# Optimization experiments

Hardware: AMD Instinct MI355X
Metric: run time of the kernel (lower is better)

Reference implementation:

```python
import jax, jax.numpy as jnp
import numpy as np


def setup_inputs() -> dict:
    key = jax.random.key(0)
    ks = jax.random.split(key, 7)
    B, S, IN, OUT = 4, 2048, 4096, 4096
    R_DEC, R_TR = 1024, 64
    return {
        "x": jax.random.normal(ks[0], (B, S, IN), dtype=jnp.float32),
        "siva_u_t": jax.random.normal(ks[1], (OUT, R_TR), dtype=jnp.float32) * 0.02,
        "siva_u_d": jax.random.normal(ks[2], (OUT, R_DEC - R_TR), dtype=jnp.float32) * 0.02,
        "siva_s": jax.random.uniform(ks[3], (R_DEC,), dtype=jnp.float32),
        "siva_v_t": jax.random.normal(ks[4], (R_TR, IN), dtype=jnp.float32) * 0.02,
        "siva_v_d": jax.random.normal(ks[5], (R_DEC - R_TR, IN), dtype=jnp.float32) * 0.02,
        "bias": jax.random.normal(ks[6], (OUT,), dtype=jnp.float32) * 0.02,
    }


def reference(x, siva_u_t, siva_u_d, siva_s, siva_v_t, siva_v_d, bias):
    # Faithful to torch: weight = (cat(U_t, U_d, dim=1) * S) @ cat(V_t, V_d, dim=0)
    siva_u = jnp.concatenate((siva_u_t, siva_u_d), axis=1)   # [out, r]
    siva_v = jnp.concatenate((siva_v_t, siva_v_d), axis=0)   # [r, in]
    weight = (siva_u * siva_s) @ siva_v                       # [out, in]
    # F.linear: x @ weight.T + bias
    return jnp.einsum("bsi,oi->bso", x, weight) + bias
```

## Files before the change

kernel.cpp:

```cpp
#include <hip/hip_runtime.h>
#include <cstdint>


typedef __bf16 bf16x8 __attribute__((ext_vector_type(8)));
typedef float f32x4 __attribute__((ext_vector_type(4)));

__device__ __forceinline__ unsigned short f32_to_bf16(float f) {
    union { float f; uint32_t u; } v; v.f = f;
    uint32_t u = v.u;
    u += 0x7FFF + ((u >> 16) & 1);
    return (unsigned short)(u >> 16);
}

__global__ void cast_f32_bf16(const float* __restrict__ src,
                              unsigned short* __restrict__ dst, int n4) {
    int i = blockIdx.x * blockDim.x + threadIdx.x;
    if (i >= n4) return;
    float4 v = ((const float4*)src)[i];
    ushort4 o;
    o.x = f32_to_bf16(v.x); o.y = f32_to_bf16(v.y);
    o.z = f32_to_bf16(v.z); o.w = f32_to_bf16(v.w);
    ((ushort4*)dst)[i] = o;
}

__global__ void build_u(const float* __restrict__ u_t, const float* __restrict__ u_d,
                        const float* __restrict__ s, unsigned short* __restrict__ ub,
                        int n4) {
    int i = blockIdx.x * blockDim.x + threadIdx.x;
    if (i >= n4) return;
    int e = i * 4;
    int o = e >> 10;
    int r = e & 1023;
    float4 u;
    if (r < 64) u = *(const float4*)(u_t + (size_t)o * 64 + r);
    else        u = *(const float4*)(u_d + (size_t)o * 960 + (r - 64));
    float4 sv = *(const float4*)(s + r);
    ushort4 w;
    w.x = f32_to_bf16(u.x * sv.x);
    w.y = f32_to_bf16(u.y * sv.y);
    w.z = f32_to_bf16(u.z * sv.z);
    w.w = f32_to_bf16(u.w * sv.w);
    ((ushort4*)ub)[i] = w;
}

__global__ void reduce_y(const float* __restrict__ p0, const float* __restrict__ p1,
                         unsigned short* __restrict__ y, int n4) {
    int i = blockIdx.x * blockDim.x + threadIdx.x;
    if (i >= n4) return;
    float4 a = ((const float4*)p0)[i];
    float4 b = ((const float4*)p1)[i];
    ushort4 w;
    w.x = f32_to_bf16(a.x + b.x);
    w.y = f32_to_bf16(a.y + b.y);
    w.z = f32_to_bf16(a.z + b.z);
    w.w = f32_to_bf16(a.w + b.w);
    ((ushort4*)y)[i] = w;
}

__device__ __forceinline__ void stage16(const unsigned short* g, unsigned short* l) {
    __builtin_amdgcn_global_load_lds(
        (const __attribute__((address_space(1))) uint32_t*)g,
        (__attribute__((address_space(3))) uint32_t*)l, 16, 0, 0);
}


#define STAGE_A(bb, kh, t_) do {                                              \
    const unsigned short* s_ = pAsrc + (t_) * 64 + (kh) * 32;                 \
    unsigned short* d_ = ldsA_dst + (bb) * 32768 + (kh) * 8192;               \
    stage16(s_, d_);                                                          \
    stage16(s_ + (size_t)128 * LD, d_ + 4096);                                \
} while (0)

#define STAGE_B(bb, kh, t_) do {                                              \
    const unsigned short* s_ = pBsrc + (t_) * 64 + (kh) * 32;                 \
    unsigned short* d_ = ldsB_dst + (bb) * 32768 + (kh) * 8192;               \
    stage16(s_, d_);                                                          \
    stage16(s_ + (size_t)128 * LD, d_ + 4096);                                \
} while (0)

#define READ_AF(bb, ks, mh) do {                                              \
    const unsigned short* p_ = lds + (bb) * 32768 + (ks) * 8192 + aoff + (mh) * 2048; \
    af[0] = *(const bf16x8*)(p_);                                             \
    af[1] = *(const bf16x8*)(p_ + 512);                                       \
    af[2] = *(const bf16x8*)(p_ + 1024);                                      \
    af[3] = *(const bf16x8*)(p_ + 1536);                                      \
} while (0)

#define READ_BF(bb, ks) do {                                                  \
    const unsigned short* p_ = lds + (bb) * 32768 + 16384 + (ks) * 8192 + boff; \
    bfr[0] = *(const bf16x8*)(p_);                                            \
    bfr[1] = *(const bf16x8*)(p_ + 512);                                      \
    bfr[2] = *(const bf16x8*)(p_ + 1024);                                     \
    bfr[3] = *(const bf16x8*)(p_ + 1536);                                     \
} while (0)

#define MFMA16(mh) do {                                                       \
    __builtin_amdgcn_s_barrier();                                             \
    __builtin_amdgcn_sched_barrier(0);                                        \
    __builtin_amdgcn_s_setprio(1);                                            \
    _Pragma("unroll") for (int i_ = 0; i_ < 4; ++i_) {                        \
        _Pragma("unroll") for (int n_ = 0; n_ < 4; ++n_) {                    \
            acc[(mh) * 4 + i_][n_] = __builtin_amdgcn_mfma_f32_16x16x32_bf16( \
                af[i_], bfr[n_], acc[(mh) * 4 + i_][n_], 0, 0, 0);            \
        }                                                                     \
    }                                                                         \
    __builtin_amdgcn_s_setprio(0);                                            \
    __builtin_amdgcn_sched_barrier(0);                                        \
} while (0)

#define PHASE_END do {                                                        \
    __builtin_amdgcn_s_barrier();                                             \
    __builtin_amdgcn_sched_barrier(0);                                        \
} while (0)

#define BODY(t_, bb) do {                                                     \
    const int tp1 = (t_) + 1, tp2 = (t_) + 2;                                 \
    bf16x8 af[4], bfr[4];                                                     \
                                                          \
    READ_AF(bb, 0, 0); READ_BF(bb, 0);                                        \
    if (tp1 < KTILES) STAGE_A((bb) ^ 1, 1, tp1);                              \
    MFMA16(0); PHASE_END;                                                     \
                                                          \
    READ_AF(bb, 0, 1);                                                        \
    if (tp1 < KTILES) STAGE_B((bb) ^ 1, 1, tp1);                              \
    MFMA16(1); PHASE_END;                                                     \
                                                          \
    READ_AF(bb, 1, 0); READ_BF(bb, 1);                                        \
    if (tp2 < KTILES) STAGE_A((bb), 0, tp2);                                  \
    MFMA16(0); PHASE_END;                                                     \
                                                          \
    READ_AF(bb, 1, 1);                                                        \
    if (tp2 < KTILES) STAGE_B((bb), 0, tp2);                                  \
    MFMA16(1);                                                                \
    if (tp2 < KTILES)      asm volatile("s_waitcnt vmcnt(4)" ::: "memory");   \
    else if (tp1 < KTILES) asm volatile("s_waitcnt vmcnt(0)" ::: "memory");   \
    PHASE_END;                                                                \
} while (0)

template<int KTILES, int LD, int NTX, bool BIAS, int SPLITK>
__global__ __launch_bounds__(512, 2)
void gemm256(const unsigned short* __restrict__ A, const unsigned short* __restrict__ B,
             float* __restrict__ C, const float* __restrict__ bias) {
    static_assert((KTILES % 2) == 0 && KTILES >= 4, "KTILES even >= 4");
    __shared__ unsigned short lds[65536];

    const int tid = threadIdx.x;
    const int wv = tid >> 6, lane = tid & 63;
    const int wm = wv >> 2, wn = wv & 3;
    const int q = lane >> 4, l16 = lane & 15;

    const int cpx = gridDim.x >> 3;
    const int bswz = (blockIdx.x & 7) * cpx + (blockIdx.x >> 3);
    const int tx = bswz % NTX, ty = bswz / NTX;
    const int m0 = ty * 256, n0 = tx * 256;

    const int z = blockIdx.z;
    const unsigned short* Az = A + (size_t)z * SPLITK;
    const unsigned short* Bz = B + (size_t)z * SPLITK;
    float* Cz = C + (size_t)z * 8192 * (NTX * 256);

    const int rowS = tid >> 2;
    const int ccS  = (tid & 3) ^ ((tid >> 3) & 3);
    const unsigned short* pAsrc = Az + (size_t)(m0 + rowS) * LD + ccS * 8;
    const unsigned short* pBsrc = Bz + (size_t)(n0 + rowS) * LD + ccS * 8;
    unsigned short* ldsA_dst = lds + tid * 8;
    unsigned short* ldsB_dst = lds + 16384 + tid * 8;

    const int xr = (l16 >> 1) & 3;
    const int qx = (q ^ xr) * 8;
    const int aoff = (wm * 128 + l16) * 32 + qx;
    const int boff = (wn * 64 + l16) * 32 + qx;

    f32x4 acc[8][4] = {};

    STAGE_A(0, 0, 0); STAGE_B(0, 0, 0);
    STAGE_A(0, 1, 0); STAGE_B(0, 1, 0);
    STAGE_A(1, 0, 1); STAGE_B(1, 0, 1);
    asm volatile("s_waitcnt vmcnt(4)" ::: "memory");
    __builtin_amdgcn_s_barrier();
    __builtin_amdgcn_sched_barrier(0);

    for (int t = 0; t < KTILES; t += 2) {
        BODY(t, 0);
        BODY(t + 1, 1);
    }

    const int ldc = NTX * 256;
    float bvv[4];
    if (BIAS) {
#pragma unroll
        for (int nf = 0; nf < 4; ++nf) bvv[nf] = bias[n0 + wn * 64 + nf * 16 + l16];
    }
#pragma unroll
    for (int mf = 0; mf < 8; ++mf) {
#pragma unroll
        for (int nf = 0; nf < 4; ++nf) {
            const int col = n0 + wn * 64 + nf * 16 + l16;
            const size_t rb = (size_t)(m0 + wm * 128 + mf * 16 + q * 4);
#pragma unroll
            for (int i = 0; i < 4; ++i) {
                float v = acc[mf][nf][i];
                if (BIAS) v += bvv[nf];
                Cz[(rb + i) * ldc + col] = v;
            }
        }
    }
}

extern "C" void kernel_launch(void* const* d_in, const int* in_sizes, int n_in,
                              void* d_out, int out_size, void* d_ws, size_t ws_size,
                              hipStream_t stream) {
    const float* x    = (const float*)d_in[0];
    const float* u_t  = (const float*)d_in[1];
    const float* u_d  = (const float*)d_in[2];
    const float* s    = (const float*)d_in[3];
    const float* v_t  = (const float*)d_in[4];
    const float* v_d  = (const float*)d_in[5];
    const float* bias = (const float*)d_in[6];
    float* out = (float*)d_out;

    const int M = 8192, IN = 4096, R = 1024, OUT = 4096;

    char* ws = (char*)d_ws;
    float*          Yp = (float*)ws;
    unsigned short* xb = (unsigned short*)(ws + (size_t)(64 << 20));
    unsigned short* Vb = (unsigned short*)(ws + (size_t)(128 << 20));
    unsigned short* Ub = (unsigned short*)(ws + (size_t)(136 << 20));
    unsigned short* Yb = (unsigned short*)(ws + (size_t)(144 << 20));

    {
        int n4 = M * IN / 4;
        cast_f32_bf16<<<(n4 + 255) / 256, 256, 0, stream>>>(x, xb, n4);
    }
    {
        int n4 = 64 * IN / 4;
        cast_f32_bf16<<<(n4 + 255) / 256, 256, 0, stream>>>(v_t, Vb, n4);
    }
    {
        int n4 = 960 * IN / 4;
        cast_f32_bf16<<<(n4 + 255) / 256, 256, 0, stream>>>(v_d, Vb + 64 * IN, n4);
    }
    {
        int n4 = OUT * R / 4;
        build_u<<<(n4 + 255) / 256, 256, 0, stream>>>(u_t, u_d, s, Ub, n4);
    }

    gemm256<32, 4096, 4, false, 2048><<<dim3(128, 1, 2), 512, 0, stream>>>(xb, Vb, Yp, nullptr);
    {
        int n4 = M * R / 4;
        reduce_y<<<(n4 + 255) / 256, 256, 0, stream>>>(Yp, Yp + (size_t)M * R, Yb, n4);
    }
    gemm256<16, 1024, 16, true, 0><<<dim3(512, 1, 1), 512, 0, stream>>>(Yb, Ub, out, bias);
}
```

Baseline: 413.9 us.

## Replace split-K first GEMM with 128x256-tile kernel writing bf16 directly

The first GEMM (x @ V^T) previously used split-K over 2 with fp32 partial outputs and a separate reduce kernel. It now uses a dedicated 128x256 tile kernel with 256 blocks over the full K, writing bf16 directly. This removes the fp32 partial round trip and one launch, and the workspace layout is compacted to match. The vmcnt wait counts in the 256-tile GEMM are also retuned so more loads stay in flight. The risks are a smaller tile with less data reuse and a waitcnt scheme that could be wrong.

```diff
diff --git a/kernel.cpp b/kernel.cpp
--- a/kernel.cpp
+++ b/kernel.cpp
@@ -43,26 +43,11 @@
     ((ushort4*)ub)[i] = w;
 }
 
-__global__ void reduce_y(const float* __restrict__ p0, const float* __restrict__ p1,
-                         unsigned short* __restrict__ y, int n4) {
-    int i = blockIdx.x * blockDim.x + threadIdx.x;
-    if (i >= n4) return;
-    float4 a = ((const float4*)p0)[i];
-    float4 b = ((const float4*)p1)[i];
-    ushort4 w;
-    w.x = f32_to_bf16(a.x + b.x);
-    w.y = f32_to_bf16(a.y + b.y);
-    w.z = f32_to_bf16(a.z + b.z);
-    w.w = f32_to_bf16(a.w + b.w);
-    ((ushort4*)y)[i] = w;
-}
-
 __device__ __forceinline__ void stage16(const unsigned short* g, unsigned short* l) {
     __builtin_amdgcn_global_load_lds(
         (const __attribute__((address_space(1))) uint32_t*)g,
         (__attribute__((address_space(3))) uint32_t*)l, 16, 0, 0);
 }
-
 
 #define STAGE_A(bb, kh, t_) do {                                              \
     const unsigned short* s_ = pAsrc + (t_) * 64 + (kh) * 32;                 \
@@ -123,7 +108,10 @@
                                                           \
     READ_AF(bb, 0, 1);                                                        \
     if (tp1 < KTILES) STAGE_B((bb) ^ 1, 1, tp1);                              \
-    MFMA16(1); PHASE_END;                                                     \
+    MFMA16(1);                                                                \
+    if (tp1 < KTILES) asm volatile("s_waitcnt vmcnt(8)" ::: "memory");        \
+    else              asm volatile("s_waitcnt vmcnt(0)" ::: "memory");        \
+    PHASE_END;                                                                \
                                                           \
     READ_AF(bb, 1, 0); READ_BF(bb, 1);                                        \
     if (tp2 < KTILES) STAGE_A((bb), 0, tp2);                                  \
@@ -132,12 +120,12 @@
     READ_AF(bb, 1, 1);                                                        \
     if (tp2 < KTILES) STAGE_B((bb), 0, tp2);                                  \
     MFMA16(1);                                                                \
-    if (tp2 < KTILES)      asm volatile("s_waitcnt vmcnt(4)" ::: "memory");   \
-    else if (tp1 < KTILES) asm volatile("s_waitcnt vmcnt(0)" ::: "memory");   \
+    if (tp2 < KTILES)      asm volatile("s_waitcnt vmcnt(8)" ::: "memory");   \
+    else if (tp1 < KTILES) asm volatile("s_waitcnt vmcnt(4)" ::: "memory");   \
     PHASE_END;                                                                \
 } while (0)
 
-template<int KTILES, int LD, int NTX, bool BIAS, int SPLITK>
+template<int KTILES, int LD, int NTX, bool BIAS>
 __global__ __launch_bounds__(512, 2)
 void gemm256(const unsigned short* __restrict__ A, const unsigned short* __restrict__ B,
              float* __restrict__ C, const float* __restrict__ bias) {
@@ -154,15 +142,10 @@
     const int tx = bswz % NTX, ty = bswz / NTX;
     const int m0 = ty * 256, n0 = tx * 256;
 
-    const int z = blockIdx.z;
-    const unsigned short* Az = A + (size_t)z * SPLITK;
-    const unsigned short* Bz = B + (size_t)z * SPLITK;
-    float* Cz = C + (size_t)z * 8192 * (NTX * 256);
-
     const int rowS = tid >> 2;
     const int ccS  = (tid & 3) ^ ((tid >> 3) & 3);
-    const unsigned short* pAsrc = Az + (size_t)(m0 + rowS) * LD + ccS * 8;
-    const unsigned short* pBsrc = Bz + (size_t)(n0 + rowS) * LD + ccS * 8;
+    const unsigned short* pAsrc = A + (size_t)(m0 + rowS) * LD + ccS * 8;
+    const unsigned short* pBsrc = B + (size_t)(n0 + rowS) * LD + ccS * 8;
     unsigned short* ldsA_dst = lds + tid * 8;
     unsigned short* ldsB_dst = lds + 16384 + tid * 8;
 
@@ -176,7 +159,7 @@
     STAGE_A(0, 0, 0); STAGE_B(0, 0, 0);
     STAGE_A(0, 1, 0); STAGE_B(0, 1, 0);
     STAGE_A(1, 0, 1); STAGE_B(1, 0, 1);
-    asm volatile("s_waitcnt vmcnt(4)" ::: "memory");
+    asm volatile("s_waitcnt vmcnt(8)" ::: "memory");
     __builtin_amdgcn_s_barrier();
     __builtin_amdgcn_sched_barrier(0);
 
@@ -201,8 +184,118 @@
             for (int i = 0; i < 4; ++i) {
                 float v = acc[mf][nf][i];
                 if (BIAS) v += bvv[nf];
-                Cz[(rb + i) * ldc + col] = v;
+                C[(rb + i) * ldc + col] = v;
             }
+        }
+    }
+}
+
+#define ST2_A(bb, kh, t_)                                                     \
+    stage16(pAsrc + (t_) * 64 + (kh) * 32, lds + (bb) * 24576 + (kh) * 4096 + tid * 8)
+
+#define ST2_B(bb, kh, t_) do {                                                \
+    const unsigned short* s_ = pBsrc + (t_) * 64 + (kh) * 32;                 \
+    unsigned short* d_ = lds + (bb) * 24576 + 8192 + (kh) * 8192 + tid * 8;   \
+    stage16(s_, d_);                                                          \
+    stage16(s_ + (size_t)128 * 4096, d_ + 4096);                              \
+} while (0)
+
+#define RD2_A(bb, ks) do {                                                    \
+    const unsigned short* p_ = lds + (bb) * 24576 + (ks) * 4096 + aoff;       \
+    af[0] = *(const bf16x8*)(p_);                                             \
+    af[1] = *(const bf16x8*)(p_ + 512);                                       \
+    af[2] = *(const bf16x8*)(p_ + 1024);                                      \
+    af[3] = *(const bf16x8*)(p_ + 1536);                                      \
+} while (0)
+
+#define RD2_B(bb, ks) do {                                                    \
+    const unsigned short* p_ = lds + (bb) * 24576 + 8192 + (ks) * 8192 + boff; \
+    bfr[0] = *(const bf16x8*)(p_);                                            \
+    bfr[1] = *(const bf16x8*)(p_ + 512);                                      \
+    bfr[2] = *(const bf16x8*)(p_ + 1024);                                     \
+    bfr[3] = *(const bf16x8*)(p_ + 1536);                                     \
+} while (0)
+
+#define MM16 do {                                                             \
+    __builtin_amdgcn_s_barrier();                                             \
+    __builtin_amdgcn_sched_barrier(0);                                        \
+    __builtin_amdgcn_s_setprio(1);                                            \
+    _Pragma("unroll") for (int i_ = 0; i_ < 4; ++i_) {                        \
+        _Pragma("unroll") for (int n_ = 0; n_ < 4; ++n_) {                    \
+            acc[i_][n_] = __builtin_amdgcn_mfma_f32_16x16x32_bf16(            \
+                af[i_], bfr[n_], acc[i_][n_], 0, 0, 0);                       \
+        }                                                                     \
+    }                                                                         \
+    __builtin_amdgcn_s_setprio(0);                                            \
+    __builtin_amdgcn_sched_barrier(0);                                        \
+} while (0)
+
+#define BODY2(t_, bb) do {                                                    \
+    const int tp1 = (t_) + 1, tp2 = (t_) + 2;                                 \
+    bf16x8 af[4], bfr[4];                                                     \
+                                                                \
+    RD2_A(bb, 0); RD2_B(bb, 0);                                               \
+    if (tp1 < 64) { ST2_A((bb) ^ 1, 1, tp1); ST2_B((bb) ^ 1, 1, tp1); }       \
+    MM16;                                                                     \
+    if (tp1 < 64) asm volatile("s_waitcnt vmcnt(6)" ::: "memory");            \
+    else          asm volatile("s_waitcnt vmcnt(0)" ::: "memory");            \
+    PHASE_END;                                                                \
+                                                                \
+    RD2_A(bb, 1); RD2_B(bb, 1);                                               \
+    if (tp2 < 64) { ST2_A((bb), 0, tp2); ST2_B((bb), 0, tp2); }               \
+    MM16;                                                                     \
+    if (tp2 < 64)      asm volatile("s_waitcnt vmcnt(6)" ::: "memory");       \
+    else if (tp1 < 64) asm volatile("s_waitcnt vmcnt(3)" ::: "memory");       \
+    PHASE_END;                                                                \
+} while (0)
+
+__global__ __launch_bounds__(512, 2)
+void gemm_a128(const unsigned short* __restrict__ A, const unsigned short* __restrict__ B,
+               unsigned short* __restrict__ Y) {
+    __shared__ unsigned short lds[49152];
+
+    const int tid = threadIdx.x;
+    const int wv = tid >> 6, lane = tid & 63;
+    const int wm = wv >> 2, wn = wv & 3;
+    const int q = lane >> 4, l16 = lane & 15;
+
+    const int bswz = (blockIdx.x & 7) * 32 + (blockIdx.x >> 3);
+    const int tx = bswz & 3, ty = bswz >> 2;
+    const int m0 = ty * 128, n0 = tx * 256;
+
+    const int rowS = tid >> 2;
+    const int ccS  = (tid & 3) ^ ((tid >> 3) & 3);
+    const unsigned short* pAsrc = A + (size_t)(m0 + rowS) * 4096 + ccS * 8;
+    const unsigned short* pBsrc = B + (size_t)(n0 + rowS) * 4096 + ccS * 8;
+
+    const int xr = (l16 >> 1) & 3;
+    const int qx = (q ^ xr) * 8;
+    const int aoff = (wm * 64 + l16) * 32 + qx;
+    const int boff = (wn * 64 + l16) * 32 + qx;
+
+    f32x4 acc[4][4] = {};
+
+    ST2_A(0, 0, 0); ST2_B(0, 0, 0);
+    ST2_A(0, 1, 0); ST2_B(0, 1, 0);
+    ST2_A(1, 0, 1); ST2_B(1, 0, 1);
+    asm volatile("s_waitcnt vmcnt(6)" ::: "memory");
+    __builtin_amdgcn_s_barrier();
+    __builtin_amdgcn_sched_barrier(0);
+
+    for (int t = 0; t < 64; t += 2) {
+        BODY2(t, 0);
+        BODY2(t + 1, 1);
+    }
+
+#pragma unroll
+    for (int mf = 0; mf < 4; ++mf) {
+#pragma unroll
+        for (int nf = 0; nf < 4; ++nf) {
+            const int col = n0 + wn * 64 + nf * 16 + l16;
+            const size_t rb = (size_t)(m0 + wm * 64 + mf * 16 + q * 4);
+#pragma unroll
+            for (int i = 0; i < 4; ++i)
+                Y[(rb + i) * 1024 + col] = f32_to_bf16(acc[mf][nf][i]);
         }
     }
 }
@@ -222,11 +315,10 @@
     const int M = 8192, IN = 4096, R = 1024, OUT = 4096;
 
     char* ws = (char*)d_ws;
-    float*          Yp = (float*)ws;
-    unsigned short* xb = (unsigned short*)(ws + (size_t)(64 << 20));
-    unsigned short* Vb = (unsigned short*)(ws + (size_t)(128 << 20));
-    unsigned short* Ub = (unsigned short*)(ws + (size_t)(136 << 20));
-    unsigned short* Yb = (unsigned short*)(ws + (size_t)(144 << 20));
+    unsigned short* xb = (unsigned short*)ws;
+    unsigned short* Vb = (unsigned short*)(ws + (size_t)(64 << 20));
+    unsigned short* Ub = (unsigned short*)(ws + (size_t)(72 << 20));
+    unsigned short* Yb = (unsigned short*)(ws + (size_t)(80 << 20));
 
     {
         int n4 = M * IN / 4;
@@ -245,10 +337,6 @@
         build_u<<<(n4 + 255) / 256, 256, 0, stream>>>(u_t, u_d, s, Ub, n4);
     }
 
-    gemm256<32, 4096, 4, false, 2048><<<dim3(128, 1, 2), 512, 0, stream>>>(xb, Vb, Yp, nullptr);
-    {
-        int n4 = M * R / 4;
-        reduce_y<<<(n4 + 255) / 256, 256, 0, stream>>>(Yp, Yp + (size_t)M * R, Yb, n4);
-    }
-    gemm256<16, 1024, 16, true, 0><<<dim3(512, 1, 1), 512, 0, stream>>>(Yb, Ub, out, bias);
-}
+    gemm_a128<<<dim3(256, 1, 1), 512, 0, stream>>>(xb, Vb, Yb);
+    gemm256<16, 1024, 16, true><<<dim3(512, 1, 1), 512, 0, stream>>>(Yb, Ub, out, bias);
+}
```

Measured after the change: 387.4 us. 1.07x faster.

## Replace split-K 256-tile GEMMs with 128-tile GEMMs and drop reduce pass

Applied to the files above, without the earlier changes.

Swaps the 256x256, 512-thread GEMM that used split-K over two partial fp32 buffers for a 128x128, 256-thread GEMM that runs the full K range and writes bf16 Y directly. This removes the reduce_y kernel and the fp32 partial-sum traffic. The second GEMM also uses the smaller tiles, giving 2048 blocks. The x cast becomes a grid-stride loop over a fixed 2048 blocks. The smaller tiles give less operand reuse per block and raise global and L2 traffic, in exchange for more blocks and fewer launches.

```diff
diff --git a/kernel.cpp b/kernel.cpp
--- a/kernel.cpp
+++ b/kernel.cpp
@@ -14,13 +14,14 @@
 
 __global__ void cast_f32_bf16(const float* __restrict__ src,
                               unsigned short* __restrict__ dst, int n4) {
-    int i = blockIdx.x * blockDim.x + threadIdx.x;
-    if (i >= n4) return;
-    float4 v = ((const float4*)src)[i];
-    ushort4 o;
-    o.x = f32_to_bf16(v.x); o.y = f32_to_bf16(v.y);
-    o.z = f32_to_bf16(v.z); o.w = f32_to_bf16(v.w);
-    ((ushort4*)dst)[i] = o;
+    for (int i = blockIdx.x * blockDim.x + threadIdx.x; i < n4;
+         i += gridDim.x * blockDim.x) {
+        float4 v = ((const float4*)src)[i];
+        ushort4 o;
+        o.x = f32_to_bf16(v.x); o.y = f32_to_bf16(v.y);
+        o.z = f32_to_bf16(v.z); o.w = f32_to_bf16(v.w);
+        ((ushort4*)dst)[i] = o;
+    }
 }
 
 __global__ void build_u(const float* __restrict__ u_t, const float* __restrict__ u_d,
@@ -43,20 +44,6 @@
     ((ushort4*)ub)[i] = w;
 }
 
-__global__ void reduce_y(const float* __restrict__ p0, const float* __restrict__ p1,
-                         unsigned short* __restrict__ y, int n4) {
-    int i = blockIdx.x * blockDim.x + threadIdx.x;
-    if (i >= n4) return;
-    float4 a = ((const float4*)p0)[i];
-    float4 b = ((const float4*)p1)[i];
-    ushort4 w;
-    w.x = f32_to_bf16(a.x + b.x);
-    w.y = f32_to_bf16(a.y + b.y);
-    w.z = f32_to_bf16(a.z + b.z);
-    w.w = f32_to_bf16(a.w + b.w);
-    ((ushort4*)y)[i] = w;
-}
-
 __device__ __forceinline__ void stage16(const unsigned short* g, unsigned short* l) {
     __builtin_amdgcn_global_load_lds(
         (const __attribute__((address_space(1))) uint32_t*)g,
@@ -64,44 +51,44 @@
 }
 
 
-#define STAGE_A(bb, kh, t_) do {                                              \
+#define ST3_A(bb, kh, t_) do {                                                \
     const unsigned short* s_ = pAsrc + (t_) * 64 + (kh) * 32;                 \
-    unsigned short* d_ = ldsA_dst + (bb) * 32768 + (kh) * 8192;               \
+    unsigned short* d_ = lds + (bb) * 8192 + (kh) * 4096 + tid * 8;           \
     stage16(s_, d_);                                                          \
-    stage16(s_ + (size_t)128 * LD, d_ + 4096);                                \
-} while (0)
-
-#define STAGE_B(bb, kh, t_) do {                                              \
+    stage16(s_ + (size_t)64 * LD, d_ + 2048);                                 \
+} while (0)
+
+#define ST3_B(bb, kh, t_) do {                                                \
     const unsigned short* s_ = pBsrc + (t_) * 64 + (kh) * 32;                 \
-    unsigned short* d_ = ldsB_dst + (bb) * 32768 + (kh) * 8192;               \
+    unsigned short* d_ = lds + 16384 + (bb) * 8192 + (kh) * 4096 + tid * 8;   \
     stage16(s_, d_);                                                          \
-    stage16(s_ + (size_t)128 * LD, d_ + 4096);                                \
-} while (0)
-
-#define READ_AF(bb, ks, mh) do {                                              \
-    const unsigned short* p_ = lds + (bb) * 32768 + (ks) * 8192 + aoff + (mh) * 2048; \
+    stage16(s_ + (size_t)64 * LD, d_ + 2048);                                 \
+} while (0)
+
+#define RD3_A(bb, kh) do {                                                    \
+    const unsigned short* p_ = lds + (bb) * 8192 + (kh) * 4096 + aoff;        \
     af[0] = *(const bf16x8*)(p_);                                             \
     af[1] = *(const bf16x8*)(p_ + 512);                                       \
     af[2] = *(const bf16x8*)(p_ + 1024);                                      \
     af[3] = *(const bf16x8*)(p_ + 1536);                                      \
 } while (0)
 
-#define READ_BF(bb, ks) do {                                                  \
-    const unsigned short* p_ = lds + (bb) * 32768 + 16384 + (ks) * 8192 + boff; \
+#define RD3_B(bb, kh) do {                                                    \
+    const unsigned short* p_ = lds + 16384 + (bb) * 8192 + (kh) * 4096 + boff; \
     bfr[0] = *(const bf16x8*)(p_);                                            \
     bfr[1] = *(const bf16x8*)(p_ + 512);                                      \
     bfr[2] = *(const bf16x8*)(p_ + 1024);                                     \
     bfr[3] = *(const bf16x8*)(p_ + 1536);                                     \
 } while (0)
 
-#define MFMA16(mh) do {                                                       \
+#define MM3 do {                                                              \
     __builtin_amdgcn_s_barrier();                                             \
     __builtin_amdgcn_sched_barrier(0);                                        \
     __builtin_amdgcn_s_setprio(1);                                            \
     _Pragma("unroll") for (int i_ = 0; i_ < 4; ++i_) {                        \
         _Pragma("unroll") for (int n_ = 0; n_ < 4; ++n_) {                    \
-            acc[(mh) * 4 + i_][n_] = __builtin_amdgcn_mfma_f32_16x16x32_bf16( \
-                af[i_], bfr[n_], acc[(mh) * 4 + i_][n_], 0, 0, 0);            \
+            acc[i_][n_] = __builtin_amdgcn_mfma_f32_16x16x32_bf16(            \
+                af[i_], bfr[n_], acc[i_][n_], 0, 0, 0);                       \
         }                                                                     \
     }                                                                         \
     __builtin_amdgcn_s_setprio(0);                                            \
@@ -113,97 +100,93 @@
     __builtin_amdgcn_sched_barrier(0);                                        \
 } while (0)
 
-#define BODY(t_, bb) do {                                                     \
+#define BODY3(t_, bb) do {                                                    \
     const int tp1 = (t_) + 1, tp2 = (t_) + 2;                                 \
     bf16x8 af[4], bfr[4];                                                     \
-                                                          \
-    READ_AF(bb, 0, 0); READ_BF(bb, 0);                                        \
-    if (tp1 < KTILES) STAGE_A((bb) ^ 1, 1, tp1);                              \
-    MFMA16(0); PHASE_END;                                                     \
-                                                          \
-    READ_AF(bb, 0, 1);                                                        \
-    if (tp1 < KTILES) STAGE_B((bb) ^ 1, 1, tp1);                              \
-    MFMA16(1); PHASE_END;                                                     \
-                                                          \
-    READ_AF(bb, 1, 0); READ_BF(bb, 1);                                        \
-    if (tp2 < KTILES) STAGE_A((bb), 0, tp2);                                  \
-    MFMA16(0); PHASE_END;                                                     \
-                                                          \
-    READ_AF(bb, 1, 1);                                                        \
-    if (tp2 < KTILES) STAGE_B((bb), 0, tp2);                                  \
-    MFMA16(1);                                                                \
-    if (tp2 < KTILES)      asm volatile("s_waitcnt vmcnt(4)" ::: "memory");   \
-    else if (tp1 < KTILES) asm volatile("s_waitcnt vmcnt(0)" ::: "memory");   \
+                                                                \
+    RD3_A(bb, 0); RD3_B(bb, 0);                                               \
+    if (tp1 < KT) { ST3_A((bb) ^ 1, 1, tp1); ST3_B((bb) ^ 1, 1, tp1); }       \
+    MM3;                                                                      \
+    if (tp1 < KT) asm volatile("s_waitcnt vmcnt(8)" ::: "memory");            \
+    else          asm volatile("s_waitcnt vmcnt(0)" ::: "memory");            \
     PHASE_END;                                                                \
-} while (0)
-
-template<int KTILES, int LD, int NTX, bool BIAS, int SPLITK>
-__global__ __launch_bounds__(512, 2)
-void gemm256(const unsigned short* __restrict__ A, const unsigned short* __restrict__ B,
-             float* __restrict__ C, const float* __restrict__ bias) {
-    static_assert((KTILES % 2) == 0 && KTILES >= 4, "KTILES even >= 4");
-    __shared__ unsigned short lds[65536];
+                                                                \
+    RD3_A(bb, 1); RD3_B(bb, 1);                                               \
+    if (tp2 < KT) { ST3_A((bb), 0, tp2); ST3_B((bb), 0, tp2); }               \
+    MM3;                                                                      \
+    if (tp2 < KT)      asm volatile("s_waitcnt vmcnt(8)" ::: "memory");       \
+    else if (tp1 < KT) asm volatile("s_waitcnt vmcnt(4)" ::: "memory");       \
+    PHASE_END;                                                                \
+} while (0)
+
+template<int KT, int LD, int NTX, bool OUTF32>
+__global__ __launch_bounds__(256, 2)
+void gemm128(const unsigned short* __restrict__ A, const unsigned short* __restrict__ B,
+             void* __restrict__ Cv, const float* __restrict__ bias) {
+    static_assert((KT % 2) == 0 && KT >= 4, "KT even >= 4");
+    __shared__ unsigned short lds[32768];
 
     const int tid = threadIdx.x;
     const int wv = tid >> 6, lane = tid & 63;
-    const int wm = wv >> 2, wn = wv & 3;
+    const int wm = wv >> 1, wn = wv & 1;
     const int q = lane >> 4, l16 = lane & 15;
 
     const int cpx = gridDim.x >> 3;
     const int bswz = (blockIdx.x & 7) * cpx + (blockIdx.x >> 3);
     const int tx = bswz % NTX, ty = bswz / NTX;
-    const int m0 = ty * 256, n0 = tx * 256;
-
-    const int z = blockIdx.z;
-    const unsigned short* Az = A + (size_t)z * SPLITK;
-    const unsigned short* Bz = B + (size_t)z * SPLITK;
-    float* Cz = C + (size_t)z * 8192 * (NTX * 256);
+    const int m0 = ty * 128, n0 = tx * 128;
 
     const int rowS = tid >> 2;
     const int ccS  = (tid & 3) ^ ((tid >> 3) & 3);
-    const unsigned short* pAsrc = Az + (size_t)(m0 + rowS) * LD + ccS * 8;
-    const unsigned short* pBsrc = Bz + (size_t)(n0 + rowS) * LD + ccS * 8;
-    unsigned short* ldsA_dst = lds + tid * 8;
-    unsigned short* ldsB_dst = lds + 16384 + tid * 8;
-
-    const int xr = (l16 >> 1) & 3;
-    const int qx = (q ^ xr) * 8;
-    const int aoff = (wm * 128 + l16) * 32 + qx;
+    const unsigned short* pAsrc = A + (size_t)(m0 + rowS) * LD + ccS * 8;
+    const unsigned short* pBsrc = B + (size_t)(n0 + rowS) * LD + ccS * 8;
+
+    const int qx = (q ^ ((l16 >> 1) & 3)) * 8;
+    const int aoff = (wm * 64 + l16) * 32 + qx;
     const int boff = (wn * 64 + l16) * 32 + qx;
 
-    f32x4 acc[8][4] = {};
-
-    STAGE_A(0, 0, 0); STAGE_B(0, 0, 0);
-    STAGE_A(0, 1, 0); STAGE_B(0, 1, 0);
-    STAGE_A(1, 0, 1); STAGE_B(1, 0, 1);
-    asm volatile("s_waitcnt vmcnt(4)" ::: "memory");
+    f32x4 acc[4][4] = {};
+
+    ST3_A(0, 0, 0); ST3_B(0, 0, 0);
+    ST3_A(0, 1, 0); ST3_B(0, 1, 0);
+    ST3_A(1, 0, 1); ST3_B(1, 0, 1);
+    asm volatile("s_waitcnt vmcnt(8)" ::: "memory");
     __builtin_amdgcn_s_barrier();
     __builtin_amdgcn_sched_barrier(0);
 
-    for (int t = 0; t < KTILES; t += 2) {
-        BODY(t, 0);
-        BODY(t + 1, 1);
-    }
-
-    const int ldc = NTX * 256;
-    float bvv[4];
-    if (BIAS) {
+    for (int t = 0; t < KT; t += 2) {
+        BODY3(t, 0);
+        BODY3(t + 1, 1);
+    }
+
+    const int ldc = NTX * 128;
+    if (OUTF32) {
+        float* C = (float*)Cv;
+        float bvv[4];
 #pragma unroll
         for (int nf = 0; nf < 4; ++nf) bvv[nf] = bias[n0 + wn * 64 + nf * 16 + l16];
-    }
-#pragma unroll
-    for (int mf = 0; mf < 8; ++mf) {
-#pragma unroll
-        for (int nf = 0; nf < 4; ++nf) {
-            const int col = n0 + wn * 64 + nf * 16 + l16;
-            const size_t rb = (size_t)(m0 + wm * 128 + mf * 16 + q * 4);
-#pragma unroll
-            for (int i = 0; i < 4; ++i) {
-                float v = acc[mf][nf][i];
-                if (BIAS) v += bvv[nf];
-                Cz[(rb + i) * ldc + col] = v;
+#pragma unroll
+        for (int mf = 0; mf < 4; ++mf)
+#pragma unroll
+            for (int nf = 0; nf < 4; ++nf) {
+                const int col = n0 + wn * 64 + nf * 16 + l16;
+                const size_t rb = (size_t)(m0 + wm * 64 + mf * 16 + q * 4);
+#pragma unroll
+                for (int i = 0; i < 4; ++i)
+                    C[(rb + i) * ldc + col] = acc[mf][nf][i] + bvv[nf];
             }
-        }
+    } else {
+        unsigned short* Y = (unsigned short*)Cv;
+#pragma unroll
+        for (int mf = 0; mf < 4; ++mf)
+#pragma unroll
+            for (int nf = 0; nf < 4; ++nf) {
+                const int col = n0 + wn * 64 + nf * 16 + l16;
+                const size_t rb = (size_t)(m0 + wm * 64 + mf * 16 + q * 4);
+#pragma unroll
+                for (int i = 0; i < 4; ++i)
+                    Y[(rb + i) * ldc + col] = f32_to_bf16(acc[mf][nf][i]);
+            }
     }
 }
 
@@ -222,15 +205,15 @@
     const int M = 8192, IN = 4096, R = 1024, OUT = 4096;
 
     char* ws = (char*)d_ws;
-    float*          Yp = (float*)ws;
-    unsigned short* xb = (unsigned short*)(ws + (size_t)(64 << 20));
-    unsigned short* Vb = (unsigned short*)(ws + (size_t)(128 << 20));
-    unsigned short* Ub = (unsigned short*)(ws + (size_t)(136 << 20));
-    unsigned short* Yb = (unsigned short*)(ws + (size_t)(144 << 20));
+    unsigned short* xb = (unsigned short*)ws;
+    unsigned short* Vb = (unsigned short*)(ws + (size_t)(64 << 20));
+    unsigned short* Ub = (unsigned short*)(ws + (size_t)(72 << 20));
+    unsigned short* Yb = (unsigned short*)(ws + (size_t)(80 << 20));
 
     {
         int n4 = M * IN / 4;
-        cast_f32_bf16<<<(n4 + 255) / 256, 256, 0, stream>>>(x, xb, n4);
+        int blocks = 2048;
+        cast_f32_bf16<<<blocks, 256, 0, stream>>>(x, xb, n4);
     }
     {
         int n4 = 64 * IN / 4;
@@ -245,10 +228,6 @@
         build_u<<<(n4 + 255) / 256, 256, 0, stream>>>(u_t, u_d, s, Ub, n4);
     }
 
-    gemm256<32, 4096, 4, false, 2048><<<dim3(128, 1, 2), 512, 0, stream>>>(xb, Vb, Yp, nullptr);
-    {
-        int n4 = M * R / 4;
-        reduce_y<<<(n4 + 255) / 256, 256, 0, stream>>>(Yp, Yp + (size_t)M * R, Yb, n4);
-    }
-    gemm256<16, 1024, 16, true, 0><<<dim3(512, 1, 1), 512, 0, stream>>>(Yb, Ub, out, bias);
-}
+    gemm128<64, 4096, 8, false><<<dim3(512, 1, 1), 256, 0, stream>>>(xb, Vb, Yb, nullptr);
+    gemm128<16, 1024, 32, true><<<dim3(2048, 1, 1), 256, 0, stream>>>(Yb, Ub, out, bias);
+}
```

Result: slower. 428.1 us (+3.4%).
